# Performance work log

Measured on AMD Instinct MI355X. Metric: run time of the kernel, lower is better.

Reference implementation:

```python
import jax, jax.numpy as jnp
import numpy as np

D_MODEL = 1024
D_HIDDEN = 4096
NUM_EXPERTS = 8
B, T = 2, 2048


def setup_inputs() -> dict:
    key = jax.random.key(0)
    ks = jax.random.split(key, 8)
    s = 0.02
    x = jax.random.normal(ks[0], (B, T, D_MODEL), dtype=jnp.float32)
    Wg = jax.random.normal(ks[1], (D_MODEL, NUM_EXPERTS), dtype=jnp.float32) * s
    bg = jnp.zeros((NUM_EXPERTS,), dtype=jnp.float32)
    W1 = jax.random.normal(ks[2], (NUM_EXPERTS, D_MODEL, D_HIDDEN), dtype=jnp.float32) * s
    b1 = jnp.zeros((NUM_EXPERTS, D_HIDDEN), dtype=jnp.float32)
    W2 = jax.random.normal(ks[3], (NUM_EXPERTS, D_HIDDEN, D_MODEL), dtype=jnp.float32) * s
    b2 = jnp.zeros((NUM_EXPERTS, D_MODEL), dtype=jnp.float32)
    return {"x": x, "Wg": Wg, "bg": bg, "W1": W1, "b1": b1, "W2": W2, "b2": b2}


def reference(x, Wg, bg, W1, b1, W2, b2):
    # Gating: top-1 routing
    gate_logits = jnp.einsum('btd,de->bte', x, Wg) + bg          # (B,T,E)
    gate_scores = jax.nn.softmax(gate_logits, axis=-1)
    top1_idx = jnp.argmax(gate_scores, axis=-1)                   # (B,T)
    top1_mask = jax.nn.one_hot(top1_idx, NUM_EXPERTS, dtype=x.dtype)  # (B,T,E)
    top1_weight = jnp.sum(gate_scores * top1_mask, axis=-1, keepdims=True)  # (B,T,1)

    # Dense all-expert compute (faithful to the naive original), then mask.
    # For unselected tokens the original computes expert(0)*0 = 0, identical
    # to expert(x)*0 = 0 here.
    h = jax.nn.silu(jnp.einsum('btd,edh->bteh', x, W1) + b1)      # (B,T,E,H)
    o = jnp.einsum('bteh,ehd->bted', h, W2) + b2                  # (B,T,E,D)
    y = jnp.sum(o * top1_mask[..., None], axis=2) * top1_weight   # (B,T,D)
    return y
```

## Files before the change

kernel.cpp:

```cpp
#include <hip/hip_runtime.h>
#include <stdint.h>

#define D_MODEL 1024
#define D_HIDDEN 4096
#define NUM_EXPERTS 8
#define NTOK 4096
#define MAXSLOT 40
#define KSPLIT 4

typedef __bf16 bf16x8 __attribute__((ext_vector_type(8)));
typedef float floatx4 __attribute__((ext_vector_type(4)));

static __device__ __forceinline__ unsigned short f2bf(float f) {
    union { float f; unsigned int i; } v;
    v.f = f;
    unsigned int i = v.i;
    unsigned int r = (i + 0x7fffu + ((i >> 16) & 1u)) >> 16;
    return (unsigned short)r;
}

__global__ __launch_bounds__(256) void gate_kernel(
    const float* __restrict__ x,
    const float* __restrict__ Wg,
    const float* __restrict__ bg,
    int* __restrict__ counts,
    int* __restrict__ tlist,
    float* __restrict__ wgt)
{
    const int wave = threadIdx.x >> 6;
    const int lane = threadIdx.x & 63;
    const int tok = blockIdx.x * 4 + wave;

    float acc[NUM_EXPERTS];
#pragma unroll
    for (int e = 0; e < NUM_EXPERTS; e++) acc[e] = 0.f;

    const float* xr = x + (size_t)tok * D_MODEL;
    for (int d = lane; d < D_MODEL; d += 64) {
        float xv = xr[d];
        const float4* wr = (const float4*)(Wg + (size_t)d * NUM_EXPERTS);
        float4 w0 = wr[0], w1 = wr[1];
        acc[0] += xv * w0.x; acc[1] += xv * w0.y;
        acc[2] += xv * w0.z; acc[3] += xv * w0.w;
        acc[4] += xv * w1.x; acc[5] += xv * w1.y;
        acc[6] += xv * w1.z; acc[7] += xv * w1.w;
    }
#pragma unroll
    for (int e = 0; e < NUM_EXPERTS; e++) {
        float v = acc[e];
#pragma unroll
        for (int off = 32; off > 0; off >>= 1) v += __shfl_xor(v, off, 64);
        acc[e] = v;
    }
    if (lane == 0) {
        float lg[NUM_EXPERTS];
#pragma unroll
        for (int e = 0; e < NUM_EXPERTS; e++) lg[e] = acc[e] + bg[e];
        int amax = 0;
        float m = lg[0];
#pragma unroll
        for (int e = 1; e < NUM_EXPERTS; e++) {
            if (lg[e] > m) { m = lg[e]; amax = e; }
        }
        float s = 0.f;
#pragma unroll
        for (int e = 0; e < NUM_EXPERTS; e++) s += __expf(lg[e] - m);
        wgt[tok] = 1.0f / s;
        int pos = atomicAdd(&counts[amax], 1);
        tlist[amax * NTOK + pos] = tok;
    }
}

__device__ __forceinline__ bool slot_to_expert(const int* counts, int slot,
                                               int& e_out, int& mt_out, int& cnt_out) {
    int cum = 0;
    for (int i = 0; i < NUM_EXPERTS; i++) {
        int c = counts[i];
        int t = (c + 127) >> 7;
        if (slot < cum + t) {
            e_out = i; mt_out = slot - cum; cnt_out = c;
            return true;
        }
        cum += t;
    }
    return false;
}

__global__ __launch_bounds__(256) void ffn1_kernel(
    const float* __restrict__ x,
    const float* __restrict__ W1,
    const float* __restrict__ b1,
    const int* __restrict__ counts,
    const int* __restrict__ tlist,
    unsigned short* __restrict__ h)
{
    int e, mt, cnt;
    if (!slot_to_expert(counts, blockIdx.y, e, mt, cnt)) return;
    const int n0 = blockIdx.x * 128;

    __shared__ __align__(16) unsigned short As[128][40];
    __shared__ __align__(16) unsigned short Bs[128][40];
    __shared__ int toks[128];

    const int tid = threadIdx.x;
    if (tid < 128) {
        int r = mt * 128 + tid;
        toks[tid] = (r < cnt) ? tlist[e * NTOK + r] : -1;
    }
    __syncthreads();

    const int wave = tid >> 6, lane = tid & 63;
    const int quad = lane >> 4, lm = lane & 15;
    const int mo = (wave & 1) * 64, no = (wave >> 1) * 64;

    floatx4 acc[4][4];
#pragma unroll
    for (int i = 0; i < 4; i++)
#pragma unroll
        for (int j = 0; j < 4; j++) acc[i][j] = (floatx4){0.f, 0.f, 0.f, 0.f};

    const float* W1e = W1 + (size_t)e * D_MODEL * D_HIDDEN;

    const int arow = tid >> 1, ahalf = tid & 1;
    int atok = toks[arow];
    const float* aptr = x + (size_t)(atok < 0 ? 0 : atok) * D_MODEL + ahalf * 16;
    const int bn = tid & 127, bg0 = tid >> 7;

    for (int k0 = 0; k0 < D_MODEL; k0 += 32) {
        float4 a4[4];
#pragma unroll
        for (int i = 0; i < 4; i++) a4[i] = ((const float4*)(aptr + k0))[i];
        unsigned short av[16];
#pragma unroll
        for (int i = 0; i < 4; i++) {
            av[i * 4 + 0] = f2bf(a4[i].x); av[i * 4 + 1] = f2bf(a4[i].y);
            av[i * 4 + 2] = f2bf(a4[i].z); av[i * 4 + 3] = f2bf(a4[i].w);
        }
        *(uint4*)(&As[arow][ahalf * 16])     = ((const uint4*)av)[0];
        *(uint4*)(&As[arow][ahalf * 16 + 8]) = ((const uint4*)av)[1];

#pragma unroll
        for (int t = 0; t < 2; t++) {
            int g = bg0 + t * 2;
            const float* bp = W1e + (size_t)(k0 + g * 8) * D_HIDDEN + n0 + bn;
            unsigned short bv[8];
#pragma unroll
            for (int j = 0; j < 8; j++) bv[j] = f2bf(bp[(size_t)j * D_HIDDEN]);
            *(uint4*)(&Bs[bn][g * 8]) = *(const uint4*)bv;
        }
        __syncthreads();

        bf16x8 af[4], bfr[4];
#pragma unroll
        for (int i = 0; i < 4; i++) {
            af[i]  = *(const bf16x8*)(&As[mo + i * 16 + lm][quad * 8]);
            bfr[i] = *(const bf16x8*)(&Bs[no + i * 16 + lm][quad * 8]);
        }
#pragma unroll
        for (int mi = 0; mi < 4; mi++)
#pragma unroll
            for (int ni = 0; ni < 4; ni++)
                acc[mi][ni] = __builtin_amdgcn_mfma_f32_16x16x32_bf16(
                    af[mi], bfr[ni], acc[mi][ni], 0, 0, 0);
        __syncthreads();
    }

    const float* b1e = b1 + (size_t)e * D_HIDDEN;
#pragma unroll
    for (int ni = 0; ni < 4; ni++) {
        int n = n0 + no + ni * 16 + lm;
        float bias = b1e[n];
#pragma unroll
        for (int mi = 0; mi < 4; mi++)
#pragma unroll
            for (int r = 0; r < 4; r++) {
                int m = mo + mi * 16 + quad * 4 + r;
                int tk = toks[m];
                if (tk >= 0) {
                    float z = acc[mi][ni][r] + bias;
                    h[(size_t)tk * D_HIDDEN + n] = f2bf(z / (1.f + __expf(-z)));
                }
            }
    }
}

__global__ __launch_bounds__(256) void ffn2_kernel(
    const unsigned short* __restrict__ h,
    const float* __restrict__ W2,
    const float* __restrict__ b2,
    const int* __restrict__ counts,
    const int* __restrict__ tlist,
    const float* __restrict__ wgt,
    float* __restrict__ out)
{
    int e, mt, cnt;
    if (!slot_to_expert(counts, blockIdx.y, e, mt, cnt)) return;
    const int n0 = blockIdx.x * 128;
    const int kc = blockIdx.z;
    const int kbeg = kc * (D_HIDDEN / KSPLIT);
    const int kend = kbeg + (D_HIDDEN / KSPLIT);

    __shared__ __align__(16) unsigned short As[128][40];
    __shared__ __align__(16) unsigned short Bs[128][40];
    __shared__ int toks[128];

    const int tid = threadIdx.x;
    if (tid < 128) {
        int r = mt * 128 + tid;
        toks[tid] = (r < cnt) ? tlist[e * NTOK + r] : -1;
    }
    __syncthreads();

    const int wave = tid >> 6, lane = tid & 63;
    const int quad = lane >> 4, lm = lane & 15;
    const int mo = (wave & 1) * 64, no = (wave >> 1) * 64;

    floatx4 acc[4][4];
#pragma unroll
    for (int i = 0; i < 4; i++)
#pragma unroll
        for (int j = 0; j < 4; j++) acc[i][j] = (floatx4){0.f, 0.f, 0.f, 0.f};

    const float* W2e = W2 + (size_t)e * D_HIDDEN * D_MODEL;

    const int arow = tid >> 1, ahalf = tid & 1;
    int atok = toks[arow];
    const unsigned short* aptr =
        h + (size_t)(atok < 0 ? 0 : atok) * D_HIDDEN + ahalf * 16;
    const int bn = tid & 127, bg0 = tid >> 7;

    for (int k0 = kbeg; k0 < kend; k0 += 32) {
        uint4 a0 = *(const uint4*)(aptr + k0);
        uint4 a1 = *(const uint4*)(aptr + k0 + 8);
        *(uint4*)(&As[arow][ahalf * 16])     = a0;
        *(uint4*)(&As[arow][ahalf * 16 + 8]) = a1;

#pragma unroll
        for (int t = 0; t < 2; t++) {
            int g = bg0 + t * 2;
            const float* bp = W2e + (size_t)(k0 + g * 8) * D_MODEL + n0 + bn;
            unsigned short bv[8];
#pragma unroll
            for (int j = 0; j < 8; j++) bv[j] = f2bf(bp[(size_t)j * D_MODEL]);
            *(uint4*)(&Bs[bn][g * 8]) = *(const uint4*)bv;
        }
        __syncthreads();

        bf16x8 af[4], bfr[4];
#pragma unroll
        for (int i = 0; i < 4; i++) {
            af[i]  = *(const bf16x8*)(&As[mo + i * 16 + lm][quad * 8]);
            bfr[i] = *(const bf16x8*)(&Bs[no + i * 16 + lm][quad * 8]);
        }
#pragma unroll
        for (int mi = 0; mi < 4; mi++)
#pragma unroll
            for (int ni = 0; ni < 4; ni++)
                acc[mi][ni] = __builtin_amdgcn_mfma_f32_16x16x32_bf16(
                    af[mi], bfr[ni], acc[mi][ni], 0, 0, 0);
        __syncthreads();
    }

    const float* b2e = b2 + (size_t)e * D_MODEL;
#pragma unroll
    for (int ni = 0; ni < 4; ni++) {
        int n = n0 + no + ni * 16 + lm;
        float bias = (kc == 0) ? b2e[n] : 0.f;
#pragma unroll
        for (int mi = 0; mi < 4; mi++)
#pragma unroll
            for (int r = 0; r < 4; r++) {
                int m = mo + mi * 16 + quad * 4 + r;
                int tk = toks[m];
                if (tk >= 0) {
                    atomicAdd(&out[(size_t)tk * D_MODEL + n],
                              (acc[mi][ni][r] + bias) * wgt[tk]);
                }
            }
    }
}

extern "C" void kernel_launch(void* const* d_in, const int* in_sizes, int n_in,
                              void* d_out, int out_size, void* d_ws, size_t ws_size,
                              hipStream_t stream) {
    const float* x  = (const float*)d_in[0];
    const float* Wg = (const float*)d_in[1];
    const float* bg = (const float*)d_in[2];
    const float* W1 = (const float*)d_in[3];
    const float* b1 = (const float*)d_in[4];
    const float* W2 = (const float*)d_in[5];
    const float* b2 = (const float*)d_in[6];
    float* out = (float*)d_out;

    char* ws = (char*)d_ws;
    int*   counts = (int*)ws;
    float* wgt    = (float*)(ws + 1024);
    int*   tlist  = (int*)(ws + 32768);
    unsigned short* h = (unsigned short*)(ws + 262144);

    hipMemsetAsync(counts, 0, NUM_EXPERTS * sizeof(int), stream);
    hipMemsetAsync(out, 0, (size_t)out_size * sizeof(float), stream);

    gate_kernel<<<NTOK / 4, 256, 0, stream>>>(x, Wg, bg, counts, tlist, wgt);
    ffn1_kernel<<<dim3(D_HIDDEN / 128, MAXSLOT), 256, 0, stream>>>(x, W1, b1, counts, tlist, h);
    ffn2_kernel<<<dim3(D_MODEL / 128, MAXSLOT, KSPLIT), 256, 0, stream>>>(h, W2, b2, counts, tlist, wgt, out);
}
```

Baseline: 574.2 us.

## Pre-transpose weights to bf16 and stage GEMM tiles via global_load_lds

Adds a prep kernel that converts W1/W2 to bf16 transposed (N-major) layouts. The gate kernel now also writes a bf16 copy of x. The FFN kernels use direct global-to-LDS 16-byte loads into an XOR-swizzled LDS layout, which removes the per-iteration strided fp32 loads and conversions. The cost is an extra full pass over both weight tensors on every call (about 268MB read) plus more workspace, and the main loop still has no double buffering.

New measurement: 592.6 us. 3.2% more time.

```diff
diff --git a/kernel.cpp b/kernel.cpp
--- a/kernel.cpp
+++ b/kernel.cpp
@@ -19,13 +19,20 @@
     return (unsigned short)r;
 }
 
+static __device__ __forceinline__ void gl_lds16(const unsigned short* g, unsigned short* l) {
+    __builtin_amdgcn_global_load_lds(
+        (const __attribute__((address_space(1))) void*)g,
+        (__attribute__((address_space(3))) void*)l, 16, 0, 0);
+}
+
 __global__ __launch_bounds__(256) void gate_kernel(
     const float* __restrict__ x,
     const float* __restrict__ Wg,
     const float* __restrict__ bg,
     int* __restrict__ counts,
     int* __restrict__ tlist,
-    float* __restrict__ wgt)
+    float* __restrict__ wgt,
+    unsigned short* __restrict__ xb)
 {
     const int wave = threadIdx.x >> 6;
     const int lane = threadIdx.x & 63;
@@ -35,15 +42,28 @@
 #pragma unroll
     for (int e = 0; e < NUM_EXPERTS; e++) acc[e] = 0.f;
 
-    const float* xr = x + (size_t)tok * D_MODEL;
-    for (int d = lane; d < D_MODEL; d += 64) {
-        float xv = xr[d];
-        const float4* wr = (const float4*)(Wg + (size_t)d * NUM_EXPERTS);
-        float4 w0 = wr[0], w1 = wr[1];
-        acc[0] += xv * w0.x; acc[1] += xv * w0.y;
-        acc[2] += xv * w0.z; acc[3] += xv * w0.w;
-        acc[4] += xv * w1.x; acc[5] += xv * w1.y;
-        acc[6] += xv * w1.z; acc[7] += xv * w1.w;
+    const float4* xr = (const float4*)(x + (size_t)tok * D_MODEL);
+    unsigned int* xbr = (unsigned int*)(xb + (size_t)tok * D_MODEL);
+
+#pragma unroll
+    for (int i = 0; i < 4; i++) {
+        int d4 = i * 64 + lane;
+        float4 v = xr[d4];
+        unsigned int p0 = (unsigned int)f2bf(v.x) | ((unsigned int)f2bf(v.y) << 16);
+        unsigned int p1 = (unsigned int)f2bf(v.z) | ((unsigned int)f2bf(v.w) << 16);
+        uint2 pk; pk.x = p0; pk.y = p1;
+        *(uint2*)&xbr[d4 * 2] = pk;
+
+        float vc[4] = {v.x, v.y, v.z, v.w};
+#pragma unroll
+        for (int c = 0; c < 4; c++) {
+            const float4* wr = (const float4*)(Wg + (size_t)(d4 * 4 + c) * NUM_EXPERTS);
+            float4 w0 = wr[0], w1 = wr[1];
+            acc[0] += vc[c] * w0.x; acc[1] += vc[c] * w0.y;
+            acc[2] += vc[c] * w0.z; acc[3] += vc[c] * w0.w;
+            acc[4] += vc[c] * w1.x; acc[5] += vc[c] * w1.y;
+            acc[6] += vc[c] * w1.z; acc[7] += vc[c] * w1.w;
+        }
     }
 #pragma unroll
     for (int e = 0; e < NUM_EXPERTS; e++) {
@@ -68,6 +88,53 @@
         wgt[tok] = 1.0f / s;
         int pos = atomicAdd(&counts[amax], 1);
         tlist[amax * NTOK + pos] = tok;
+    }
+}
+
+__global__ __launch_bounds__(256) void prep_kernel(
+    const float* __restrict__ W1, const float* __restrict__ W2,
+    unsigned short* __restrict__ w1t, unsigned short* __restrict__ w2t)
+{
+    const int t = blockIdx.x;
+    const float* src; unsigned short* dst;
+    int R, C, r0, c0;
+    if (t < 8192) {
+        int e = t >> 10, ti = t & 1023;
+        R = D_MODEL; C = D_HIDDEN;
+        r0 = (ti >> 6) * 64; c0 = (ti & 63) * 64;
+        src = W1 + (size_t)e * D_MODEL * D_HIDDEN;
+        dst = w1t + (size_t)e * D_MODEL * D_HIDDEN;
+    } else {
+        int t2 = t - 8192;
+        int e = t2 >> 10, ti = t2 & 1023;
+        R = D_HIDDEN; C = D_MODEL;
+        r0 = (ti >> 4) * 64; c0 = (ti & 15) * 64;
+        src = W2 + (size_t)e * D_MODEL * D_HIDDEN;
+        dst = w2t + (size_t)e * D_MODEL * D_HIDDEN;
+    }
+
+    __shared__ unsigned short T[64][66];
+    const int tid = threadIdx.x;
+    {
+        const int lr = tid >> 4, cq = tid & 15;
+#pragma unroll
+        for (int i = 0; i < 4; i++) {
+            float4 v = *(const float4*)(src + (size_t)(r0 + lr + i * 16) * C + c0 + cq * 4);
+            unsigned int p0 = (unsigned int)f2bf(v.x) | ((unsigned int)f2bf(v.y) << 16);
+            unsigned int p1 = (unsigned int)f2bf(v.z) | ((unsigned int)f2bf(v.w) << 16);
+            *(unsigned int*)&T[lr + i * 16][cq * 4]     = p0;
+            *(unsigned int*)&T[lr + i * 16][cq * 4 + 2] = p1;
+        }
+    }
+    __syncthreads();
+    {
+        const int oc = tid >> 2, oj = tid & 3;
+        __attribute__((aligned(16))) unsigned short vals[16];
+#pragma unroll
+        for (int j = 0; j < 16; j++) vals[j] = T[oj * 16 + j][oc];
+        unsigned short* orow = dst + (size_t)(c0 + oc) * R + r0 + oj * 16;
+        *(uint4*)(orow)     = ((const uint4*)vals)[0];
+        *(uint4*)(orow + 8) = ((const uint4*)vals)[1];
     }
 }
 
@@ -76,19 +143,19 @@
     int cum = 0;
     for (int i = 0; i < NUM_EXPERTS; i++) {
         int c = counts[i];
-        int t = (c + 127) >> 7;
-        if (slot < cum + t) {
+        int tt = (c + 127) >> 7;
+        if (slot < cum + tt) {
             e_out = i; mt_out = slot - cum; cnt_out = c;
             return true;
         }
-        cum += t;
+        cum += tt;
     }
     return false;
 }
 
 __global__ __launch_bounds__(256) void ffn1_kernel(
-    const float* __restrict__ x,
-    const float* __restrict__ W1,
+    const unsigned short* __restrict__ xb,
+    const unsigned short* __restrict__ w1t,
     const float* __restrict__ b1,
     const int* __restrict__ counts,
     const int* __restrict__ tlist,
@@ -98,8 +165,8 @@
     if (!slot_to_expert(counts, blockIdx.y, e, mt, cnt)) return;
     const int n0 = blockIdx.x * 128;
 
-    __shared__ __align__(16) unsigned short As[128][40];
-    __shared__ __align__(16) unsigned short Bs[128][40];
+    __shared__ __align__(16) unsigned short As[128 * 32];
+    __shared__ __align__(16) unsigned short Bs[128 * 32];
     __shared__ int toks[128];
 
     const int tid = threadIdx.x;
@@ -113,48 +180,39 @@
     const int quad = lane >> 4, lm = lane & 15;
     const int mo = (wave & 1) * 64, no = (wave >> 1) * 64;
 
+    const int srow = wave * 16 + (lane >> 2);
+    const int kq = (lane & 3) ^ ((lane >> 3) & 3);
+    int tA0 = toks[srow], tA1 = toks[64 + srow];
+    const unsigned short* a0p = xb + (size_t)(tA0 < 0 ? 0 : tA0) * D_MODEL + kq * 8;
+    const unsigned short* a1p = xb + (size_t)(tA1 < 0 ? 0 : tA1) * D_MODEL + kq * 8;
+    const unsigned short* w1e = w1t + (size_t)e * D_HIDDEN * D_MODEL;
+    const unsigned short* b0p = w1e + (size_t)(n0 + srow) * D_MODEL + kq * 8;
+    const unsigned short* b1p = w1e + (size_t)(n0 + 64 + srow) * D_MODEL + kq * 8;
+    unsigned short* Ad0 = As + wave * 512;
+    unsigned short* Ad1 = As + 2048 + wave * 512;
+    unsigned short* Bd0 = Bs + wave * 512;
+    unsigned short* Bd1 = Bs + 2048 + wave * 512;
+
+    const int fq = (quad ^ ((lm >> 1) & 3)) * 8;
+
     floatx4 acc[4][4];
 #pragma unroll
     for (int i = 0; i < 4; i++)
 #pragma unroll
         for (int j = 0; j < 4; j++) acc[i][j] = (floatx4){0.f, 0.f, 0.f, 0.f};
 
-    const float* W1e = W1 + (size_t)e * D_MODEL * D_HIDDEN;
-
-    const int arow = tid >> 1, ahalf = tid & 1;
-    int atok = toks[arow];
-    const float* aptr = x + (size_t)(atok < 0 ? 0 : atok) * D_MODEL + ahalf * 16;
-    const int bn = tid & 127, bg0 = tid >> 7;
-
     for (int k0 = 0; k0 < D_MODEL; k0 += 32) {
-        float4 a4[4];
-#pragma unroll
-        for (int i = 0; i < 4; i++) a4[i] = ((const float4*)(aptr + k0))[i];
-        unsigned short av[16];
+        gl_lds16(a0p + k0, Ad0);
+        gl_lds16(a1p + k0, Ad1);
+        gl_lds16(b0p + k0, Bd0);
+        gl_lds16(b1p + k0, Bd1);
+        __syncthreads();
+
+        bf16x8 af[4], bfr[4];
 #pragma unroll
         for (int i = 0; i < 4; i++) {
-            av[i * 4 + 0] = f2bf(a4[i].x); av[i * 4 + 1] = f2bf(a4[i].y);
-            av[i * 4 + 2] = f2bf(a4[i].z); av[i * 4 + 3] = f2bf(a4[i].w);
-        }
-        *(uint4*)(&As[arow][ahalf * 16])     = ((const uint4*)av)[0];
-        *(uint4*)(&As[arow][ahalf * 16 + 8]) = ((const uint4*)av)[1];
-
-#pragma unroll
-        for (int t = 0; t < 2; t++) {
-            int g = bg0 + t * 2;
-            const float* bp = W1e + (size_t)(k0 + g * 8) * D_HIDDEN + n0 + bn;
-            unsigned short bv[8];
-#pragma unroll
-            for (int j = 0; j < 8; j++) bv[j] = f2bf(bp[(size_t)j * D_HIDDEN]);
-            *(uint4*)(&Bs[bn][g * 8]) = *(const uint4*)bv;
-        }
-        __syncthreads();
-
-        bf16x8 af[4], bfr[4];
-#pragma unroll
-        for (int i = 0; i < 4; i++) {
-            af[i]  = *(const bf16x8*)(&As[mo + i * 16 + lm][quad * 8]);
-            bfr[i] = *(const bf16x8*)(&Bs[no + i * 16 + lm][quad * 8]);
+            af[i]  = *(const bf16x8*)(As + (mo + i * 16 + lm) * 32 + fq);
+            bfr[i] = *(const bf16x8*)(Bs + (no + i * 16 + lm) * 32 + fq);
         }
 #pragma unroll
         for (int mi = 0; mi < 4; mi++)
@@ -186,7 +244,7 @@
 
 __global__ __launch_bounds__(256) void ffn2_kernel(
     const unsigned short* __restrict__ h,
-    const float* __restrict__ W2,
+    const unsigned short* __restrict__ w2t,
     const float* __restrict__ b2,
     const int* __restrict__ counts,
     const int* __restrict__ tlist,
@@ -198,10 +256,9 @@
     const int n0 = blockIdx.x * 128;
     const int kc = blockIdx.z;
     const int kbeg = kc * (D_HIDDEN / KSPLIT);
-    const int kend = kbeg + (D_HIDDEN / KSPLIT);
-
-    __shared__ __align__(16) unsigned short As[128][40];
-    __shared__ __align__(16) unsigned short Bs[128][40];
+
+    __shared__ __align__(16) unsigned short As[128 * 32];
+    __shared__ __align__(16) unsigned short Bs[128 * 32];
     __shared__ int toks[128];
 
     const int tid = threadIdx.x;
@@ -215,42 +272,39 @@
     const int quad = lane >> 4, lm = lane & 15;
     const int mo = (wave & 1) * 64, no = (wave >> 1) * 64;
 
+    const int srow = wave * 16 + (lane >> 2);
+    const int kq = (lane & 3) ^ ((lane >> 3) & 3);
+    int tA0 = toks[srow], tA1 = toks[64 + srow];
+    const unsigned short* a0p = h + (size_t)(tA0 < 0 ? 0 : tA0) * D_HIDDEN + kbeg + kq * 8;
+    const unsigned short* a1p = h + (size_t)(tA1 < 0 ? 0 : tA1) * D_HIDDEN + kbeg + kq * 8;
+    const unsigned short* w2e = w2t + (size_t)e * D_MODEL * D_HIDDEN;
+    const unsigned short* b0p = w2e + (size_t)(n0 + srow) * D_HIDDEN + kbeg + kq * 8;
+    const unsigned short* b1p = w2e + (size_t)(n0 + 64 + srow) * D_HIDDEN + kbeg + kq * 8;
+    unsigned short* Ad0 = As + wave * 512;
+    unsigned short* Ad1 = As + 2048 + wave * 512;
+    unsigned short* Bd0 = Bs + wave * 512;
+    unsigned short* Bd1 = Bs + 2048 + wave * 512;
+
+    const int fq = (quad ^ ((lm >> 1) & 3)) * 8;
+
     floatx4 acc[4][4];
 #pragma unroll
     for (int i = 0; i < 4; i++)
 #pragma unroll
         for (int j = 0; j < 4; j++) acc[i][j] = (floatx4){0.f, 0.f, 0.f, 0.f};
 
-    const float* W2e = W2 + (size_t)e * D_HIDDEN * D_MODEL;
-
-    const int arow = tid >> 1, ahalf = tid & 1;
-    int atok = toks[arow];
-    const unsigned short* aptr =
-        h + (size_t)(atok < 0 ? 0 : atok) * D_HIDDEN + ahalf * 16;
-    const int bn = tid & 127, bg0 = tid >> 7;
-
-    for (int k0 = kbeg; k0 < kend; k0 += 32) {
-        uint4 a0 = *(const uint4*)(aptr + k0);
-        uint4 a1 = *(const uint4*)(aptr + k0 + 8);
-        *(uint4*)(&As[arow][ahalf * 16])     = a0;
-        *(uint4*)(&As[arow][ahalf * 16 + 8]) = a1;
-
-#pragma unroll
-        for (int t = 0; t < 2; t++) {
-            int g = bg0 + t * 2;
-            const float* bp = W2e + (size_t)(k0 + g * 8) * D_MODEL + n0 + bn;
-            unsigned short bv[8];
-#pragma unroll
-            for (int j = 0; j < 8; j++) bv[j] = f2bf(bp[(size_t)j * D_MODEL]);
-            *(uint4*)(&Bs[bn][g * 8]) = *(const uint4*)bv;
-        }
+    for (int k0 = 0; k0 < D_HIDDEN / KSPLIT; k0 += 32) {
+        gl_lds16(a0p + k0, Ad0);
+        gl_lds16(a1p + k0, Ad1);
+        gl_lds16(b0p + k0, Bd0);
+        gl_lds16(b1p + k0, Bd1);
         __syncthreads();
 
         bf16x8 af[4], bfr[4];
 #pragma unroll
         for (int i = 0; i < 4; i++) {
-            af[i]  = *(const bf16x8*)(&As[mo + i * 16 + lm][quad * 8]);
-            bfr[i] = *(const bf16x8*)(&Bs[no + i * 16 + lm][quad * 8]);
+            af[i]  = *(const bf16x8*)(As + (mo + i * 16 + lm) * 32 + fq);
+            bfr[i] = *(const bf16x8*)(Bs + (no + i * 16 + lm) * 32 + fq);
         }
 #pragma unroll
         for (int mi = 0; mi < 4; mi++)
@@ -296,12 +350,16 @@
     int*   counts = (int*)ws;
     float* wgt    = (float*)(ws + 1024);
     int*   tlist  = (int*)(ws + 32768);
-    unsigned short* h = (unsigned short*)(ws + 262144);
+    unsigned short* xb   = (unsigned short*)(ws + 262144);
+    unsigned short* hbuf = (unsigned short*)(ws + 8650752);
+    unsigned short* w1t  = (unsigned short*)(ws + 42205184);
+    unsigned short* w2t  = (unsigned short*)(ws + 109314048);
 
     hipMemsetAsync(counts, 0, NUM_EXPERTS * sizeof(int), stream);
     hipMemsetAsync(out, 0, (size_t)out_size * sizeof(float), stream);
 
-    gate_kernel<<<NTOK / 4, 256, 0, stream>>>(x, Wg, bg, counts, tlist, wgt);
-    ffn1_kernel<<<dim3(D_HIDDEN / 128, MAXSLOT), 256, 0, stream>>>(x, W1, b1, counts, tlist, h);
-    ffn2_kernel<<<dim3(D_MODEL / 128, MAXSLOT, KSPLIT), 256, 0, stream>>>(h, W2, b2, counts, tlist, wgt, out);
-}
+    prep_kernel<<<16384, 256, 0, stream>>>(W1, W2, w1t, w2t);
+    gate_kernel<<<NTOK / 4, 256, 0, stream>>>(x, Wg, bg, counts, tlist, wgt, xb);
+    ffn1_kernel<<<dim3(D_HIDDEN / 128, MAXSLOT), 256, 0, stream>>>(xb, w1t, b1, counts, tlist, hbuf);
+    ffn2_kernel<<<dim3(D_MODEL / 128, MAXSLOT, KSPLIT), 256, 0, stream>>>(hbuf, w2t, b2, counts, tlist, wgt, out);
+}
```
